# Performance work log

Hardware: AMD Instinct MI355X
Metric: run time of the kernel (lower is better)

Reference implementation:

```python
import jax, jax.numpy as jnp
import numpy as np

B, N = 1, 6
CIN, CIMG, DD = 256, 80, 59
FH, FW, IH, IW = 32, 88, 256, 704
XY0, DXY, NX = -54.0, 0.3, 360
Z0, DZ, NZ = -10.0, 20.0, 1
NPTS = B * N * DD * FH * FW


def _conv(x, w, stride, pad, b=None):
    y = jax.lax.conv_general_dilated(x, w, (stride, stride), ((pad, pad), (pad, pad)),
                                     dimension_numbers=('NCHW', 'OIHW', 'NCHW'))
    return y if b is None else y + b[None, :, None, None]


def _bnrelu(x, s, t):
    # eval-mode BatchNorm folded into per-channel scale/shift, then ReLU
    return jax.nn.relu(x * s[None, :, None, None] + t[None, :, None, None])


def _frustum():
    ds = jnp.arange(1.0, 60.0, 1.0)                      # D = 59 depth bins
    xs = jnp.linspace(0.0, IW - 1.0, FW)
    ys = jnp.linspace(0.0, IH - 1.0, FH)
    dm = jnp.broadcast_to(ds[:, None, None], (DD, FH, FW))
    xm = jnp.broadcast_to(xs[None, None, :], (DD, FH, FW))
    ym = jnp.broadcast_to(ys[None, :, None], (DD, FH, FW))
    return jnp.stack([xm, ym, dm], -1)                   # [D,FH,FW,3]


def _fwd(x_img, d, cam2lidar_rots, cam2lidar_trans, intrins, post_rots, post_trans,
         dt1_w, dt1_b, dt1_s, dt1_t, dt2_w, dt2_b, dt2_s, dt2_t, dt3_w, dt3_b, dt3_s, dt3_t,
         dn1_w, dn1_b, dn1_s, dn1_t, dn2_w, dn2_b, dn2_s, dn2_t, dn3_w, dn3_b,
         ds1_w, ds1_s, ds1_t, ds2_w, ds2_s, ds2_t):
    # ---- get_cam_feats: dtransform on raw depth, concat, depthnet ----
    h = _bnrelu(_conv(d.reshape(B * N, 1, IH, IW), dt1_w, 1, 0, dt1_b), dt1_s, dt1_t)
    h = _bnrelu(_conv(h, dt2_w, 4, 2, dt2_b), dt2_s, dt2_t)
    h = _bnrelu(_conv(h, dt3_w, 2, 2, dt3_b), dt3_s, dt3_t)      # [BN,64,FH,FW]
    f = jnp.concatenate([h, x_img], 1)                           # [BN,320,FH,FW]
    f = _bnrelu(_conv(f, dn1_w, 1, 1, dn1_b), dn1_s, dn1_t)
    f = _bnrelu(_conv(f, dn2_w, 1, 1, dn2_b), dn2_s, dn2_t)
    f = _conv(f, dn3_w, 1, 0, dn3_b)                             # [BN,D+C,FH,FW]
    depth = jax.nn.softmax(f[:, :DD], axis=1)                    # [BN,D,FH,FW]
    cam = depth[:, None] * f[:, DD:DD + CIMG][:, :, None]        # [BN,C,D,FH,FW]
    cam = cam.reshape(B, N, CIMG, DD, FH, FW).transpose(0, 1, 3, 4, 5, 2)  # [B,N,D,FH,FW,C]
    # ---- get_geometry ----
    fr = _frustum()
    pts = fr[None, None] - post_trans[:, :, None, None, None, :]
    pts = jnp.einsum('bnij,bndhwj->bndhwi', jnp.linalg.inv(post_rots), pts)
    pts = jnp.concatenate([pts[..., :2] * pts[..., 2:3], pts[..., 2:3]], -1)
    comb = jnp.einsum('bnij,bnjk->bnik', cam2lidar_rots, jnp.linalg.inv(intrins))
    pts = jnp.einsum('bnij,bndhwj->bndhwi', comb, pts) + cam2lidar_trans[:, :, None, None, None, :]
    # ---- bev_pool: voxelize + scatter-sum ----
    lo = jnp.array([XY0, XY0, Z0], dtype=pts.dtype)
    dxv = jnp.array([DXY, DXY, DZ], dtype=pts.dtype)
    g = ((pts - lo) / dxv).astype(jnp.int32).reshape(-1, 3)      # trunc-toward-zero like torch .long()
    feats = cam.reshape(-1, CIMG)
    kept = (g[:, 0] >= 0) & (g[:, 0] < NX) & (g[:, 1] >= 0) & (g[:, 1] < NX) & (g[:, 2] >= 0) & (g[:, 2] < NZ)
    bix = jnp.repeat(jnp.arange(B), NPTS // B)
    flat = ((bix * NZ + g[:, 2]) * NX + g[:, 0]) * NX + g[:, 1]
    flat = jnp.where(kept, flat, 0)
    feats = jnp.where(kept[:, None], feats, jnp.zeros((), feats.dtype))
    pooled = jax.ops.segment_sum(feats, flat, num_segments=B * NZ * NX * NX)
    # [B,Z,X,Y,C] -> [B,Z*C,X,Y] (z-major channel concat, matches cat(unbind(dim=2)))
    bev = pooled.reshape(B, NZ, NX, NX, CIMG).transpose(0, 1, 4, 2, 3).reshape(B, NZ * CIMG, NX, NX)
    # ---- downsample block (stride 2) ----
    y = _bnrelu(_conv(bev, ds1_w, 2, 1), ds1_s, ds1_t)
    y = _bnrelu(_conv(y, ds2_w, 1, 1), ds2_s, ds2_t)             # [B,80,180,180]
    return y


def setup_inputs() -> dict:
    k = jax.random.split(jax.random.key(0), 40)
    w = lambda i, s: (0.05 * jax.random.normal(k[i], s)).astype(jnp.float32)
    sc = lambda i, c: (1.0 + 0.01 * jax.random.normal(k[i], (c,))).astype(jnp.float32)
    eye = jnp.broadcast_to(jnp.eye(3, dtype=jnp.float32), (B, N, 3, 3))
    Rcl = jnp.broadcast_to(jnp.array([[0., 0., 1.], [-1., 0., 0.], [0., -1., 0.]], dtype=jnp.float32), (B, N, 3, 3))
    K = jnp.broadcast_to(jnp.array([[560., 0., 352.], [0., 560., 128.], [0., 0., 1.]], dtype=jnp.float32), (B, N, 3, 3))
    return dict(
        x_img=jax.random.normal(k[0], (B * N, CIN, FH, FW), dtype=jnp.float32),
        d=60.0 * jax.random.uniform(k[1], (B, N, 1, IH, IW), dtype=jnp.float32),
        cam2lidar_rots=Rcl + 0.005 * jax.random.normal(k[2], (B, N, 3, 3)),
        cam2lidar_trans=0.5 * jax.random.normal(k[3], (B, N, 3)),
        intrins=K,
        post_rots=eye + 0.001 * jax.random.normal(k[4], (B, N, 3, 3)),
        post_trans=jnp.zeros((B, N, 3), jnp.float32),
        dt1_w=w(5, (8, 1, 1, 1)), dt1_b=w(6, (8,)), dt1_s=sc(7, 8), dt1_t=w(8, (8,)),
        dt2_w=w(9, (32, 8, 5, 5)), dt2_b=w(10, (32,)), dt2_s=sc(11, 32), dt2_t=w(12, (32,)),
        dt3_w=w(13, (64, 32, 5, 5)), dt3_b=w(14, (64,)), dt3_s=sc(15, 64), dt3_t=w(16, (64,)),
        dn1_w=w(17, (256, 320, 3, 3)), dn1_b=w(18, (256,)), dn1_s=sc(19, 256), dn1_t=w(20, (256,)),
        dn2_w=w(21, (256, 256, 3, 3)), dn2_b=w(22, (256,)), dn2_s=sc(23, 256), dn2_t=w(24, (256,)),
        dn3_w=w(25, (139, 256, 1, 1)), dn3_b=w(26, (139,)),
        ds1_w=w(27, (80, 80, 3, 3)), ds1_s=sc(28, 80), ds1_t=w(29, (80,)),
        ds2_w=w(30, (80, 80, 3, 3)), ds2_s=sc(31, 80), ds2_t=w(32, (80,)),
    )


def reference(x_img, d, cam2lidar_rots, cam2lidar_trans, intrins, post_rots, post_trans,
              dt1_w, dt1_b, dt1_s, dt1_t, dt2_w, dt2_b, dt2_s, dt2_t, dt3_w, dt3_b, dt3_s, dt3_t,
              dn1_w, dn1_b, dn1_s, dn1_t, dn2_w, dn2_b, dn2_s, dn2_t, dn3_w, dn3_b,
              ds1_w, ds1_s, ds1_t, ds2_w, ds2_s, ds2_t):
    return _fwd(x_img, d, cam2lidar_rots, cam2lidar_trans, intrins, post_rots, post_trans,
                dt1_w, dt1_b, dt1_s, dt1_t, dt2_w, dt2_b, dt2_s, dt2_t, dt3_w, dt3_b, dt3_s, dt3_t,
                dn1_w, dn1_b, dn1_s, dn1_t, dn2_w, dn2_b, dn2_s, dn2_t, dn3_w, dn3_b,
                ds1_w, ds1_s, ds1_t, ds2_w, ds2_s, ds2_t)
```

## Files before the change

### kernel.cpp

```cpp
#include <hip/hip_runtime.h>
#include <math.h>

#define NCAM 6
#define IH 256
#define IW 704
#define FH 32
#define FW 88
#define DD 59
#define CIMG 80
#define NXv 360
#define PIX (FH*FW)
#define IMGPIX (IH*IW)
#define NPTS (NCAM*DD*PIX)
#define NCELLS (NXv*NXv)
#define NB 127
#define UNIT 32
#define MAXUNITS (NCELLS + NPTS/UNIT + 1)
#define GATHER_BLOCKS ((MAXUNITS + 3) / 4)

#define MPITCH 96
#define MROWS  35
#define MSLAB  (MROWS*MPITCH)

#define DP_R 260
#define DP_C 708
#define H2_R 68
#define H2_C 180

#define DSM   32400
#define DSP1  362
#define DSP2  182
#define DSC   96

typedef _Float16 f16;
typedef f16  f16x8 __attribute__((ext_vector_type(8)));
typedef float f32x4 __attribute__((ext_vector_type(4)));

#define SWZ(r, g) (((r)<<5) + (((g) ^ ((r)&3))<<3))

#define OFF_MATS 0
#define OFF_WDS1 144
#define OFF_WDT2 34704
#define OFF_WDS2 57744
#define OFF_A    115344
#define OFF_DNH  OFF_A
#define OFF_H2NH (OFF_A + 4416960)
#define OFF_Q3   OFF_A
#define OFF_Q2   (OFF_A + 4325376)
#define OFF_WT1  (OFF_A + 6905856)
#define OFF_WT2  (OFF_A + 7274496)
#define OFF_TD3  (OFF_A + 7569408)
#define OFF_B    10483344
#define OFF_WDT3 OFF_B
#define OFF_CNT    (OFF_B)
#define OFF_INCL   (OFF_B + 131072)
#define OFF_OFFS   (OFF_B + 262144)
#define OFF_CURSOR (OFF_B + 393216)
#define OFF_BSUM   (OFF_B + 524288)
#define OFF_UCNT   (OFF_B + 524480)
#define OFF_BSX    (OFF_B + 524544)
#define OFF_UNITS  (OFF_B + 525312)
#define OFF_POOLH  (OFF_B)
#define OFF_BEV1H  (OFF_B + 6289632)
#define OFF_C    12831888
#define OFF_D      13913232
#define OFF_Q1     OFF_D
#define OFF_FEATT  OFF_D
#define OFF_FLAT   (OFF_D + 1351680)
#define OFF_ORDYX  (OFF_D + 2348544)
#define OFF_ORDD   (OFF_D + 3345408)


__device__ __forceinline__ void inv3(const float* m, float* o) {
    float a=m[0],b=m[1],c=m[2],d=m[3],e=m[4],f=m[5],g=m[6],h=m[7],i=m[8];
    float A =  (e*i - f*h);
    float B = -(d*i - f*g);
    float C =  (d*h - e*g);
    float det = a*A + b*B + c*C;
    float r = 1.f/det;
    o[0]=A*r;            o[1]=-(b*i - c*h)*r; o[2]=(b*f - c*e)*r;
    o[3]=B*r;            o[4]=(a*i - c*g)*r;  o[5]=-(a*f - c*d)*r;
    o[6]=C*r;            o[7]=-(a*h - b*g)*r; o[8]=(a*e - b*d)*r;
}

__global__ void k_cam_mats(const float* __restrict__ prot, const float* __restrict__ ptran,
                           const float* __restrict__ intr, const float* __restrict__ Rcl,
                           const float* __restrict__ tcl, float* __restrict__ mats) {
    int n = threadIdx.x;
    if (n >= NCAM) return;
    float P[9], Km[9], R[9], A[9], Ki[9];
    for (int i=0;i<9;i++){ P[i]=prot[n*9+i]; Km[i]=intr[n*9+i]; R[i]=Rcl[n*9+i]; }
    inv3(P, A); inv3(Km, Ki);
    float* M = mats + n*24;
    for (int i=0;i<9;i++) M[i] = A[i];
    for (int r=0;r<3;r++)
        M[9+r] = -(A[r*3+0]*ptran[n*3+0] + A[r*3+1]*ptran[n*3+1] + A[r*3+2]*ptran[n*3+2]);
    for (int r=0;r<3;r++) for (int c=0;c<3;c++)
        M[12 + r*3+c] = R[r*3+0]*Ki[0*3+c] + R[r*3+1]*Ki[1*3+c] + R[r*3+2]*Ki[2*3+c];
    for (int r=0;r<3;r++) M[21+r] = tcl[n*3+r];
}

__global__ void k_wtrans_ds(const float* __restrict__ w, f16* __restrict__ Wt) {
    int i = blockIdx.x*blockDim.x + threadIdx.x;
    if (i >= 3*80*288) return;
    int k  = i % 288;
    int co = (i / 288) % 80;
    int kx = i / (288*80);
    int ky = k / 96, ci = k % 96;
    Wt[i] = (ci < 80) ? (f16)w[((co*80 + ci)*3 + kx)*3 + ky] : (f16)0.f;
}

__global__ void k_wtrans_dt2(const float* __restrict__ w, f16* __restrict__ Wt) {
    int i = blockIdx.x*blockDim.x + threadIdx.x;
    if (i >= 5*32*64) return;
    int ky = i / (32*64);
    int r  = i % (32*64);
    int co = r / 64;
    int k  = r % 64;
    int kx = k / 8, ci = k % 8;
    Wt[i] = (kx < 5) ? (f16)w[co*200 + ci*25 + ky*5 + kx] : (f16)0.f;
}

__global__ void k_wtrans_dt3(const float* __restrict__ w, f16* __restrict__ Wt) {
    int i = blockIdx.x*blockDim.x + threadIdx.x;
    if (i >= 5*64*160) return;
    int ky = i / (64*160);
    int r  = i % (64*160);
    int co = r / 160;
    int k  = r % 160;
    int kx = k / 32, ci = k % 32;
    Wt[i] = (f16)w[co*800 + ci*25 + ky*5 + kx];
}

__global__ void k_prep_b3(const float* __restrict__ w, f16* __restrict__ Wt) {
    int i = blockIdx.x*blockDim.x + threadIdx.x;
    if (i >= 144*256) return;
    int co = i / 256;
    Wt[i] = (co < 139) ? (f16)w[i] : (f16)0.f;
}

template<int CIN>
__global__ void k_prep_b(const float* __restrict__ w, f16* __restrict__ Wt) {
    int co = blockIdx.x;
    int ci = threadIdx.x;
    const float* src = w + ((size_t)co*CIN + ci)*9;
    #pragma unroll
    for (int t=0;t<9;t++)
        Wt[((size_t)t*256 + co)*CIN + ci] = (f16)src[t];
}

__global__ __launch_bounds__(256) void k_prep_d(const float* __restrict__ d,
                                                const float* __restrict__ w,
                                                const float* __restrict__ b,
                                                const float* __restrict__ s,
                                                const float* __restrict__ t,
                                                f16* __restrict__ dNH) {
    int i = blockIdx.x*256 + threadIdx.x;
    int cam = i / IMGPIX;
    int yx = i % IMGPIX;
    int y = yx / IW, x = yx % IW;
    float v = d[i];
    f16* dst = dNH + ((size_t)cam*DP_R + (y+2))*DP_C*8 + (size_t)(x+2)*8;
    #pragma unroll
    for (int c=0;c<8;c++)
        dst[c] = (f16)fmaxf(fmaf(fmaf(v, w[c], b[c]), s[c], t[c]), 0.f);
}

__global__ __launch_bounds__(256) void k_gemm_dt2(const f16* __restrict__ dNH,
                                                  const f16* __restrict__ Wt,
                                                  const float* __restrict__ bias,
                                                  const float* __restrict__ bn_s,
                                                  const float* __restrict__ bn_t,
                                                  f16* __restrict__ h2NH) {
    __shared__ f16 lA[128*32];
    __shared__ f16 lB[32*32];
    int cam = blockIdx.x / 88, mt = blockIdx.x % 88;
    int m0 = mt*128;
    int tid = threadIdx.x;
    int wid = tid>>6, lane = tid&63;
    int wm = wid*32;
    int lr = lane&15, quad = lane>>4;
    int swr = ((quad ^ (lr&3))<<3);
    f32x4 acc[2][2] = {};

    int rr = tid >> 1;
    int g0 = tid & 1, g1 = g0 + 2;
    int am = m0 + rr;
    int ay = am / 176, ax = am % 176;
    const f16* abase = dNH + (size_t)cam*DP_R*DP_C*8 + (size_t)(ay*4)*DP_C*8 + (size_t)(ax*4)*8;

    for (int ky=0; ky<5; ky++) {
        const f16* arow = abase + (size_t)ky*DP_C*8;
        const f16* brow = Wt + ((size_t)ky*32 + rr)*64;
        #pragma unroll
        for (int k0=0; k0<64; k0+=32) {
            *(float4*)(&lA[SWZ(rr,g0)]) = *(const float4*)(arow + k0 + g0*8);
            *(float4*)(&lA[SWZ(rr,g1)]) = *(const float4*)(arow + k0 + g1*8);
            if (tid < 64) {
                *(float4*)(&lB[SWZ(rr,g0)]) = *(const float4*)(brow + k0 + g0*8);
                *(float4*)(&lB[SWZ(rr,g1)]) = *(const float4*)(brow + k0 + g1*8);
            }
            __syncthreads();
            f16x8 af[2], bf[2];
            #pragma unroll
            for (int i=0;i<2;i++) af[i] = *(f16x8*)(&lA[((wm+i*16+lr)<<5) + swr]);
            #pragma unroll
            for (int j=0;j<2;j++) bf[j] = *(f16x8*)(&lB[((j*16+lr)<<5) + swr]);
            #pragma unroll
            for (int i=0;i<2;i++)
                #pragma unroll
                for (int j=0;j<2;j++)
                    acc[i][j] = __builtin_amdgcn_mfma_f32_16x16x32_f16(af[i], bf[j], acc[i][j], 0,0,0);
            __syncthreads();
        }
    }
    #pragma unroll
    for (int j=0;j<2;j++) {
        int n = j*16 + lr;
        float bb = bias[n], ss = bn_s[n], tt = bn_t[n];
        #pragma unroll
        for (int i=0;i<2;i++) {
            #pragma unroll
            for (int r=0;r<4;r++) {
                int m = m0 + wm + i*16 + quad*4 + r;
                int y = m / 176, x = m % 176;
                float v = fmaxf(fmaf(acc[i][j][r] + bb, ss, tt), 0.f);
                h2NH[((size_t)cam*H2_R + (y+2))*H2_C*32 + (size_t)(x+2)*32 + n] = (f16)v;
            }
        }
    }
}

__global__ __launch_bounds__(256) void k_gemm_dt3(const f16* __restrict__ h2NH,
                                                  const f16* __restrict__ Wt,
                                                  const float* __restrict__ bias,
                                                  const float* __restrict__ bn_s,
                                                  const float* __restrict__ bn_t,
                                                  f16* __restrict__ Q1) {
    __shared__ f16 lA[128*32];
    __shared__ f16 lB[64*32];
    int cam = blockIdx.x / 22, mt = blockIdx.x % 22;
    int m0 = mt*128;
    int tid = threadIdx.x;
    int wid = tid>>6, lane = tid&63;
    int wm = wid*32;
    int lr = lane&15, quad = lane>>4;
    int swr = ((quad ^ (lr&3))<<3);
    f32x4 acc[2][4] = {};

    int rr = tid >> 1;
    int g0 = tid & 1, g1 = g0 + 2;
    int am = m0 + rr;
    int ay = am / FW, ax = am % FW;
    const f16* abase = h2NH + (size_t)cam*H2_R*H2_C*32 + (size_t)(ay*2)*H2_C*32 + (size_t)(ax*2)*32;

    for (int ky=0; ky<5; ky++) {
        const f16* arow = abase + (size_t)ky*H2_C*32;
        const f16* brow = Wt + ((size_t)ky*64 + rr)*160;
        #pragma unroll
        for (int k0=0; k0<160; k0+=32) {
            *(float4*)(&lA[SWZ(rr,g0)]) = *(const float4*)(arow + k0 + g0*8);
            *(float4*)(&lA[SWZ(rr,g1)]) = *(const float4*)(arow + k0 + g1*8);
            if (tid < 128) {
                *(float4*)(&lB[SWZ(rr,g0)]) = *(const float4*)(brow + k0 + g0*8);
                *(float4*)(&lB[SWZ(rr,g1)]) = *(const float4*)(brow + k0 + g1*8);
            }
            __syncthreads();
            f16x8 af[2], bf[4];
            #pragma unroll
            for (int i=0;i<2;i++) af[i] = *(f16x8*)(&lA[((wm+i*16+lr)<<5) + swr]);
            #pragma unroll
            for (int j=0;j<4;j++) bf[j] = *(f16x8*)(&lB[((j*16+lr)<<5) + swr]);
            #pragma unroll
            for (int i=0;i<2;i++)
                #pragma unroll
                for (int j=0;j<4;j++)
                    acc[i][j] = __builtin_amdgcn_mfma_f32_16x16x32_f16(af[i], bf[j], acc[i][j], 0,0,0);
            __syncthreads();
        }
    }
    #pragma unroll
    for (int j=0;j<4;j++) {
        int n = j*16 + lr;
        float bb = bias[n], ss = bn_s[n], tt = bn_t[n];
        #pragma unroll
        for (int i=0;i<2;i++) {
            #pragma unroll
            for (int r=0;r<4;r++) {
                int m = m0 + wm + i*16 + quad*4 + r;
                int y = m / FW, x = m % FW;
                float v = fmaxf(fmaf(acc[i][j][r] + bb, ss, tt), 0.f);
                Q1[((size_t)cam*MSLAB + (size_t)(y+1)*MPITCH + (x+1))*320 + n] = (f16)v;
            }
        }
    }
}

__global__ __launch_bounds__(256) void k_prep_a1x(const float* __restrict__ x_img,
                                                  f16* __restrict__ Q1) {
    __shared__ f16 tile[88*260];
    int y = blockIdx.x, cam = blockIdx.y;
    for (int e = threadIdx.x; e < 88*256; e += 256) {
        int c = e / 88, p = e % 88;
        tile[p*260 + c] = (f16)x_img[((size_t)cam*256 + c)*PIX + y*FW + p];
    }
    __syncthreads();
    f16* dst = Q1 + (size_t)cam*(MSLAB*320) + ((size_t)(y+1)*MPITCH + 1)*320 + 64;
    for (int e = threadIdx.x; e < 88*256; e += 256) {
        int p = e / 256, c = e % 256;
        dst[(size_t)p*320 + c] = tile[p*260 + c];
    }
}

template<int KCI, int EPI>
__global__ __launch_bounds__(256) void k_gemm_conv(const f16* __restrict__ Aq,
                                                   const f16* __restrict__ Wt,
                                                   const float* __restrict__ bias,
                                                   const float* __restrict__ bn_s,
                                                   const float* __restrict__ bn_t,
                                                   f16* __restrict__ outh) {
    __shared__ f16 lA[128*32];
    __shared__ f16 lB[128*32];
    int cam = blockIdx.x / 24, mt = blockIdx.x % 24;
    int m0 = mt*128;
    int co0 = blockIdx.y * 128;
    int tid = threadIdx.x;
    f32x4 acc[4][4] = {};
    const f16* Abase = Aq + (size_t)cam*MSLAB*KCI;
    int rr = tid >> 1;
    int g0 = tid & 1, g1 = g0 + 2;
    int wid = tid>>6, lane = tid&63;
    int wm = (wid&1)*64, wn = (wid>>1)*64;
    int lr = lane&15, quad = lane>>4;
    int swr = ((quad ^ (lr&3))<<3);

    for (int t=0; t<9; t++) {
        int moff = (t/3)*MPITCH + (t%3);
        const f16* At = Abase + (size_t)(m0 + moff + rr)*KCI;
        const f16* Bt = Wt + ((size_t)t*256 + co0 + rr)*KCI;
        for (int k0=0; k0<KCI; k0+=32) {
            *(float4*)(&lA[SWZ(rr,g0)]) = *(const float4*)(At + k0 + g0*8);
            *(float4*)(&lA[SWZ(rr,g1)]) = *(const float4*)(At + k0 + g1*8);
            *(float4*)(&lB[SWZ(rr,g0)]) = *(const float4*)(Bt + k0 + g0*8);
            *(float4*)(&lB[SWZ(rr,g1)]) = *(const float4*)(Bt + k0 + g1*8);
            __syncthreads();
            f16x8 af[4], bf[4];
            #pragma unroll
            for (int i=0;i<4;i++) af[i] = *(f16x8*)(&lA[((wm+i*16+lr)<<5) + swr]);
            #pragma unroll
            for (int j=0;j<4;j++) bf[j] = *(f16x8*)(&lB[((wn+j*16+lr)<<5) + swr]);
            #pragma unroll
            for (int i=0;i<4;i++)
                #pragma unroll
                for (int j=0;j<4;j++)
                    acc[i][j] = __builtin_amdgcn_mfma_f32_16x16x32_f16(af[i], bf[j], acc[i][j], 0,0,0);
            __syncthreads();
        }
    }
    #pragma unroll
    for (int j=0;j<4;j++) {
        int n = co0 + wn + j*16 + lr;
        float bb = bias[n], ss = bn_s[n], tt = bn_t[n];
        #pragma unroll
        for (int i=0;i<4;i++) {
            #pragma unroll
            for (int r=0;r<4;r++) {
                int m = m0 + wm + i*16 + quad*4 + r;
                int y = m / MPITCH, x = m % MPITCH;
                if (x >= FW || y >= FH) continue;
                float v = fmaxf(fmaf(acc[i][j][r] + bb, ss, tt), 0.f);
                if (EPI == 0)
                    outh[((size_t)cam*MSLAB + (size_t)(y+1)*MPITCH + (x+1))*256 + n] = (f16)v;
                else
                    outh[((size_t)cam*PIX + (size_t)(y*FW + x))*256 + n] = (f16)v;
            }
        }
    }
}

__global__ __launch_bounds__(256) void k_gemm_dn3(const f16* __restrict__ Q3,
                                                  const f16* __restrict__ Wt,
                                                  const float* __restrict__ bias,
                                                  float* __restrict__ f3) {
    __shared__ f16 lA[128*32];
    __shared__ f16 lB[144*32];
    int cam = blockIdx.x / 22, mt = blockIdx.x % 22;
    int m0 = mt*128;
    int tid = threadIdx.x;
    int wid = tid>>6, lane = tid&63;
    int wm = wid*32;
    int lr = lane&15, quad = lane>>4;
    int swr = ((quad ^ (lr&3))<<3);
    f32x4 acc[2][9] = {};

    int rr = tid >> 1;
    int g0 = tid & 1, g1 = g0 + 2;
    const f16* abase = Q3 + ((size_t)cam*PIX + m0 + rr)*256;
    const f16* bbase = Wt + (size_t)tid*256;

    for (int k0=0; k0<256; k0+=32) {
        *(float4*)(&lA[SWZ(rr,g0)]) = *(const float4*)(abase + k0 + g0*8);
        *(float4*)(&lA[SWZ(rr,g1)]) = *(const float4*)(abase + k0 + g1*8);
        if (tid < 144) {
            #pragma unroll
            for (int g=0; g<4; g++)
                *(float4*)(&lB[SWZ(tid,g)]) = *(const float4*)(bbase + k0 + g*8);
        }
        __syncthreads();
        f16x8 af[2], bf[9];
        #pragma unroll
        for (int i=0;i<2;i++) af[i] = *(f16x8*)(&lA[((wm+i*16+lr)<<5) + swr]);
        #pragma unroll
        for (int j=0;j<9;j++) bf[j] = *(f16x8*)(&lB[((j*16+lr)<<5) + swr]);
        #pragma unroll
        for (int i=0;i<2;i++)
            #pragma unroll
            for (int j=0;j<9;j++)
                acc[i][j] = __builtin_amdgcn_mfma_f32_16x16x32_f16(af[i], bf[j], acc[i][j], 0,0,0);
        __syncthreads();
    }
    #pragma unroll
    for (int j=0;j<9;j++) {
        int n = j*16 + lr;
        if (n >= 139) continue;
        float bb = bias[n];
        #pragma unroll
        for (int i=0;i<2;i++) {
            #pragma unroll
            for (int r=0;r<4;r++) {
                int m = m0 + wm + i*16 + quad*4 + r;
                f3[((size_t)cam*139 + n)*PIX + m] = acc[i][j][r] + bb;
            }
        }
    }
}

__global__ __launch_bounds__(256) void k_softmax_feat(const float* __restrict__ f3,
                                                      float* __restrict__ depth,
                                                      float* __restrict__ featT) {
    int o = blockIdx.x*256 + threadIdx.x;
    int n = o / PIX, yx = o % PIX;
    const float* fp = f3 + (size_t)n*139*PIX + yx;
    float m = -1e30f;
    for (int d=0; d<DD; d++) m = fmaxf(m, fp[(size_t)d*PIX]);
    float sum = 0.f;
    for (int d=0; d<DD; d++) sum += expf(fp[(size_t)d*PIX]-m);
    float inv = 1.f/sum;
    for (int d=0; d<DD; d++)
        depth[((size_t)n*DD+d)*PIX + yx] = expf(fp[(size_t)d*PIX]-m)*inv;
    float* ft = featT + (size_t)o*CIMG;
    for (int c=0; c<CIMG; c++) ft[c] = fp[(size_t)(DD+c)*PIX];
}

__global__ __launch_bounds__(256) void k_voxel(const float* __restrict__ mats, int* __restrict__ flat,
                                               int* __restrict__ cnt) {
    int p = blockIdx.x*256 + threadIdx.x;
    if (p >= NPTS) return;
    int x = p % FW; int t1 = p / FW;
    int y = t1 % FH; int t2 = t1 / FH;
    int dd = t2 % DD; int n = t2 / DD;
    float xf = x * (703.f/87.f);
    float yf = y * (255.f/31.f);
    float df = 1.f + (float)dd;
    const float* M = mats + n*24;
    float qx = M[0]*xf + M[1]*yf + M[2]*df + M[9];
    float qy = M[3]*xf + M[4]*yf + M[5]*df + M[10];
    float qz = M[6]*xf + M[7]*yf + M[8]*df + M[11];
    float rx = qx*qz, ry = qy*qz, rz = qz;
    float wx = M[12]*rx + M[13]*ry + M[14]*rz + M[21];
    float wy = M[15]*rx + M[16]*ry + M[17]*rz + M[22];
    float wz = M[18]*rx + M[19]*ry + M[20]*rz + M[23];
    int gx = (int)((wx + 54.f) / 0.3f);
    int gy = (int)((wy + 54.f) / 0.3f);
    int gz = (int)((wz + 10.f) / 20.f);
    bool kept = ((unsigned)gx < NXv) && ((unsigned)gy < NXv) && (gz == 0);
    int cell = kept ? (gx*NXv + gy) : -1;
    flat[p] = cell;
    if (kept) atomicAdd(&cnt[cell], 1);
}

__global__ __launch_bounds__(256) void k_scan1(const int* __restrict__ cnt, int* __restrict__ incl,
                                               int* __restrict__ bsum) {
    int tid = threadIdx.x;
    int idx = blockIdx.x*1024 + tid*4;
    int c0 = (idx+0 < NCELLS) ? cnt[idx+0] : 0;
    int c1 = (idx+1 < NCELLS) ? cnt[idx+1] : 0;
    int c2 = (idx+2 < NCELLS) ? cnt[idx+2] : 0;
    int c3 = (idx+3 < NCELLS) ? cnt[idx+3] : 0;
    int s0=c0, s1=s0+c1, s2=s1+c2, s3=s2+c3;
    int v = s3;
    int lane = tid & 63, wid = tid >> 6;
    #pragma unroll
    for (int d=1; d<64; d<<=1) {
        int u = __shfl_up(v, d, 64);
        if (lane >= d) v += u;
    }
    __shared__ int wsum[4];
    if (lane == 63) wsum[wid] = v;
    __syncthreads();
    int woff = 0;
    #pragma unroll
    for (int w=0; w<3; w++) if (w < wid) woff += wsum[w];
    int texcl = woff + v - s3;
    if (idx+0 < NCELLS) incl[idx+0] = texcl + s0;
    if (idx+1 < NCELLS) incl[idx+1] = texcl + s1;
    if (idx+2 < NCELLS) incl[idx+2] = texcl + s2;
    if (idx+3 < NCELLS) incl[idx+3] = texcl + s3;
    if (tid == 255) bsum[blockIdx.x] = woff + v;
}

__global__ void k_scan2(const int* __restrict__ bsum, int* __restrict__ bsx,
                        int* __restrict__ ucount) {
    int lane = threadIdx.x;
    if (lane == 0) *ucount = 0;
    int a = (2*lane   < NB) ? bsum[2*lane]   : 0;
    int b = (2*lane+1 < NB) ? bsum[2*lane+1] : 0;
    int s = a + b;
    int v = s;
    #pragma unroll
    for (int d=1; d<64; d<<=1) {
        int u = __shfl_up(v, d, 64);
        if (lane >= d) v += u;
    }
    int excl = v - s;
    if (2*lane   < NB) bsx[2*lane]   = excl;
    if (2*lane+1 < NB) bsx[2*lane+1] = excl + a;
}

__global__ __launch_bounds__(256) void k_scan3(const int* __restrict__ incl, const int* __restrict__ cnt,
                                               const int* __restrict__ bsx, int* __restrict__ offs,
                                               int* __restrict__ cursor,
                                               int* __restrict__ units, int* __restrict__ ucount) {
    int idx = blockIdx.x*1024 + threadIdx.x*4;
    int o = bsx[blockIdx.x];
    #pragma unroll
    for (int j=0;j<4;j++) {
        int cell = idx + j;
        if (cell < NCELLS) {
            int k = cnt[cell];
            int e = o + incl[cell] - k;
            offs[cell] = e;
            cursor[cell] = e;
            if (k > 0) {
                int nu = (k + UNIT-1) / UNIT;
                int ub = atomicAdd(ucount, nu);
                int multi = (nu > 1) ? (1<<17) : 0;
                for (int u=0; u<nu; u++) {
                    int c2 = min(UNIT, k - u*UNIT);
                    units[2*(ub+u)]   = cell | multi | (c2<<18);
                    units[2*(ub+u)+1] = e + u*UNIT;
                }
            }
        }
    }
}

__global__ __launch_bounds__(256) void k_fill(const int* __restrict__ flat, int* __restrict__ cursor,
                                              const float* __restrict__ depth,
                                              int* __restrict__ ordYX, float* __restrict__ ordD) {
    int p = blockIdx.x*256 + threadIdx.x;
    if (p >= NPTS) return;
    int cell = flat[p];
    if (cell < 0) return;
    int pos = atomicAdd(&cursor[cell], 1);
    int n = p / (DD*PIX);
    int yx = p % PIX;
    ordYX[pos] = n*PIX + yx;
    ordD[pos] = depth[p];
}

__global__ __launch_bounds__(256) void k_gather2(const int* __restrict__ units,
                                                 const int* __restrict__ ucount,
                                                 const int* __restrict__ ordYX,
                                                 const float* __restrict__ ordD,
                                                 const float* __restrict__ featT,
                                                 float* __restrict__ pooled) {
    int idx = blockIdx.x*4 + (threadIdx.x >> 6);
    if (idx >= *ucount) return;
    int lane = threadIdx.x & 63;
    int u0 = units[2*idx], base = units[2*idx+1];
    int cell = u0 & 0x1ffff;
    bool multi = (u0 >> 17) & 1;
    int count = u0 >> 18;
    float acc0 = 0.f, acc1 = 0.f;
    bool lo = (lane < 16);
    int i = 0;
    for (; i+2 <= count; i += 2) {
        int y0 = ordYX[base+i], y1 = ordYX[base+i+1];
        float d0 = ordD[base+i], d1 = ordD[base+i+1];
        const float* f0 = featT + (size_t)y0*CIMG;
        const float* f1 = featT + (size_t)y1*CIMG;
        float a = f0[lane];
        float b = f1[lane];
        float c = lo ? f0[64+lane] : 0.f;
        float d = lo ? f1[64+lane] : 0.f;
        acc0 = fmaf(d0, a, acc0);
        acc0 = fmaf(d1, b, acc0);
        acc1 = fmaf(d0, c, acc1);
        acc1 = fmaf(d1, d, acc1);
    }
    if (i < count) {
        int y0 = ordYX[base+i];
        float d0 = ordD[base+i];
        const float* f0 = featT + (size_t)y0*CIMG;
        acc0 = fmaf(d0, f0[lane], acc0);
        if (lo) acc1 = fmaf(d0, f0[64+lane], acc1);
    }
    float* dst = pooled + (size_t)cell*CIMG;
    if (multi) {
        atomicAdd(dst + lane, acc0);
        if (lo) atomicAdd(dst + 64 + lane, acc1);
    } else {
        dst[lane] = acc0;
        if (lo) dst[64 + lane] = acc1;
    }
}

__global__ __launch_bounds__(256) void k_pool2h(const float* __restrict__ pooled,
                                                f16* __restrict__ pooledH) {
    int gx = blockIdx.x;
    const float* src = pooled + (size_t)gx*360*80;
    for (int e = threadIdx.x; e < 360*80; e += 256) {
        int gy = e / 80, c = e % 80;
        pooledH[((size_t)(gx+1)*DSP1 + (gy+1))*DSC + c] = (f16)src[e];
    }
}

template<int STRIDE, int HINP, int EPI>
__global__ __launch_bounds__(256) void k_ds_mfma(const f16* __restrict__ inH,
                                                 const f16* __restrict__ Wt,
                                                 const float* __restrict__ bn_s,
                                                 const float* __restrict__ bn_t,
                                                 f16* __restrict__ outh,
                                                 float* __restrict__ outf) {
    __shared__ f16 lA[128*32];
    __shared__ f16 lB[80*32];
    int m0 = blockIdx.x * 128;
    int tid = threadIdx.x;
    int wid = tid>>6, lane = tid&63;
    int wm = wid*32;
    int lr = lane&15, quad = lane>>4;
    int swr = ((quad ^ (lr&3))<<3);
    f32x4 acc[2][5] = {};

    int rr = tid >> 1;
    int g0 = tid & 1, g1 = g0 + 2;
    int am = min(m0 + rr, DSM-1);
    int axo = am / 180, ayo = am % 180;
    const f16* arow0 = inH + ((size_t)(axo*STRIDE)*HINP + (size_t)ayo*STRIDE)*DSC;
    const f16* brow0 = Wt + (size_t)rr*288;

    for (int kx=0; kx<3; kx++) {
        const f16* arow = arow0 + (size_t)kx*HINP*DSC;
        const f16* brow = brow0 + (size_t)kx*80*288;
        for (int k0=0; k0<288; k0+=32) {
            *(float4*)(&lA[SWZ(rr,g0)]) = *(const float4*)(arow + k0 + g0*8);
            *(float4*)(&lA[SWZ(rr,g1)]) = *(const float4*)(arow + k0 + g1*8);
            if (tid < 160) {
                *(float4*)(&lB[SWZ(rr,g0)]) = *(const float4*)(brow + k0 + g0*8);
                *(float4*)(&lB[SWZ(rr,g1)]) = *(const float4*)(brow + k0 + g1*8);
            }
            __syncthreads();
            f16x8 af[2], bf[5];
            #pragma unroll
            for (int i=0;i<2;i++) af[i] = *(f16x8*)(&lA[((wm+i*16+lr)<<5) + swr]);
            #pragma unroll
            for (int j=0;j<5;j++) bf[j] = *(f16x8*)(&lB[((j*16+lr)<<5) + swr]);
            #pragma unroll
            for (int i=0;i<2;i++)
                #pragma unroll
                for (int j=0;j<5;j++)
                    acc[i][j] = __builtin_amdgcn_mfma_f32_16x16x32_f16(af[i], bf[j], acc[i][j], 0,0,0);
            __syncthreads();
        }
    }
    #pragma unroll
    for (int j=0;j<5;j++) {
        int n = j*16 + lr;
        float ss = bn_s[n], tt = bn_t[n];
        #pragma unroll
        for (int i=0;i<2;i++) {
            #pragma unroll
            for (int r=0;r<4;r++) {
                int m = m0 + wm + i*16 + quad*4 + r;
                if (m >= DSM) continue;
                float v = fmaxf(fmaf(acc[i][j][r], ss, tt), 0.f);
                if (EPI == 0) {
                    int xo = m / 180, yo = m % 180;
                    outh[((size_t)(xo+1)*DSP2 + (yo+1))*DSC + n] = (f16)v;
                } else {
                    outf[(size_t)n*DSM + m] = v;
                }
            }
        }
    }
}

extern "C" void kernel_launch(void* const* d_in, const int* in_sizes, int n_in,
                              void* d_out, int out_size, void* d_ws, size_t ws_size,
                              hipStream_t stream) {
    const float* x_img  = (const float*)d_in[0];
    const float* dimg   = (const float*)d_in[1];
    const float* c2l_R  = (const float*)d_in[2];
    const float* c2l_t  = (const float*)d_in[3];
    const float* intr   = (const float*)d_in[4];
    const float* prot   = (const float*)d_in[5];
    const float* ptran  = (const float*)d_in[6];
    const float* dt1_w  = (const float*)d_in[7];
    const float* dt1_b  = (const float*)d_in[8];
    const float* dt1_s  = (const float*)d_in[9];
    const float* dt1_t  = (const float*)d_in[10];
    const float* dt2_w  = (const float*)d_in[11];
    const float* dt2_b  = (const float*)d_in[12];
    const float* dt2_s  = (const float*)d_in[13];
    const float* dt2_t  = (const float*)d_in[14];
    const float* dt3_w  = (const float*)d_in[15];
    const float* dt3_b  = (const float*)d_in[16];
    const float* dt3_s  = (const float*)d_in[17];
    const float* dt3_t  = (const float*)d_in[18];
    const float* dn1_w  = (const float*)d_in[19];
    const float* dn1_b  = (const float*)d_in[20];
    const float* dn1_s  = (const float*)d_in[21];
    const float* dn1_t  = (const float*)d_in[22];
    const float* dn2_w  = (const float*)d_in[23];
    const float* dn2_b  = (const float*)d_in[24];
    const float* dn2_s  = (const float*)d_in[25];
    const float* dn2_t  = (const float*)d_in[26];
    const float* dn3_w  = (const float*)d_in[27];
    const float* dn3_b  = (const float*)d_in[28];
    const float* ds1_w  = (const float*)d_in[29];
    const float* ds1_s  = (const float*)d_in[30];
    const float* ds1_t  = (const float*)d_in[31];
    const float* ds2_w  = (const float*)d_in[32];
    const float* ds2_s  = (const float*)d_in[33];
    const float* ds2_t  = (const float*)d_in[34];

    float* ws = (float*)d_ws;
    float* mats   = ws + OFF_MATS;
    f16*   WtDS1  = (f16*)(ws + OFF_WDS1);
    f16*   WtDS2  = (f16*)(ws + OFF_WDS2);
    f16*   WtDT2  = (f16*)(ws + OFF_WDT2);
    f16*   WtDT3  = (f16*)(ws + OFF_WDT3);
    f16*   dNH    = (f16*)(ws + OFF_DNH);
    f16*   h2NH   = (f16*)(ws + OFF_H2NH);
    f16*   Q3     = (f16*)(ws + OFF_Q3);
    float* pooled = ws + OFF_A;
    f16*   Q2     = (f16*)(ws + OFF_Q2);
    f16*   Wt1    = (f16*)(ws + OFF_WT1);
    f16*   Wt2    = (f16*)(ws + OFF_WT2);
    f16*   Wt3h   = (f16*)(ws + OFF_TD3);
    float* f3     = ws + OFF_B;
    int*   cnt    = (int*)(ws + OFF_CNT);
    int*   incl   = (int*)(ws + OFF_INCL);
    int*   offs   = (int*)(ws + OFF_OFFS);
    int*   cursor = (int*)(ws + OFF_CURSOR);
    int*   bsum   = (int*)(ws + OFF_BSUM);
    int*   ucnt   = (int*)(ws + OFF_UCNT);
    int*   bsx    = (int*)(ws + OFF_BSX);
    int*   units  = (int*)(ws + OFF_UNITS);
    f16*   pooledH= (f16*)(ws + OFF_POOLH);
    f16*   bev1H  = (f16*)(ws + OFF_BEV1H);
    float* depth  = ws + OFF_C;
    f16*   Q1     = (f16*)(ws + OFF_Q1);
    float* featT  = ws + OFF_FEATT;
    int*   flat   = (int*)(ws + OFF_FLAT);
    int*   ordYX  = (int*)(ws + OFF_ORDYX);
    float* ordD   = ws + OFF_ORDD;
    float* outp   = (float*)d_out;

    k_cam_mats<<<1, 64, 0, stream>>>(prot, ptran, intr, c2l_R, c2l_t, mats);
    k_wtrans_ds<<<270, 256, 0, stream>>>(ds1_w, WtDS1);
    k_wtrans_ds<<<270, 256, 0, stream>>>(ds2_w, WtDS2);
    k_wtrans_dt2<<<40, 256, 0, stream>>>(dt2_w, WtDT2);
    k_wtrans_dt3<<<200, 256, 0, stream>>>(dt3_w, WtDT3);
    k_prep_b3<<<144, 256, 0, stream>>>(dn3_w, Wt3h);
    k_prep_b<320><<<256, 320, 0, stream>>>(dn1_w, Wt1);
    k_prep_b<256><<<256, 256, 0, stream>>>(dn2_w, Wt2);

    hipMemsetAsync(dNH, 0, (size_t)NCAM*DP_R*DP_C*8*sizeof(f16), stream);
    hipMemsetAsync(h2NH, 0, (size_t)NCAM*H2_R*H2_C*32*sizeof(f16), stream);
    hipMemsetAsync(Q1, 0, (size_t)NCAM*MSLAB*320*sizeof(f16), stream);

    k_prep_d<<<4224, 256, 0, stream>>>(dimg, dt1_w, dt1_b, dt1_s, dt1_t, dNH);
    k_gemm_dt2<<<528, 256, 0, stream>>>(dNH, WtDT2, dt2_b, dt2_s, dt2_t, h2NH);
    k_gemm_dt3<<<132, 256, 0, stream>>>(h2NH, WtDT3, dt3_b, dt3_s, dt3_t, Q1);
    k_prep_a1x<<<dim3(32,NCAM), 256, 0, stream>>>(x_img, Q1);

    hipMemsetAsync(Q2, 0, (size_t)NCAM*MSLAB*256*sizeof(f16), stream);
    k_gemm_conv<320,0><<<dim3(144,2), 256, 0, stream>>>(Q1, Wt1, dn1_b, dn1_s, dn1_t, Q2);
    k_gemm_conv<256,1><<<dim3(144,2), 256, 0, stream>>>(Q2, Wt2, dn2_b, dn2_s, dn2_t, Q3);
    k_gemm_dn3<<<132, 256, 0, stream>>>(Q3, Wt3h, dn3_b, f3);

    k_softmax_feat<<<66, 256, 0, stream>>>(f3, depth, featT);

    hipMemsetAsync(cnt, 0, NCELLS*sizeof(int), stream);
    hipMemsetAsync(pooled, 0, (size_t)NCELLS*CIMG*sizeof(float), stream);
    k_voxel<<<3894, 256, 0, stream>>>(mats, flat, cnt);
    k_scan1<<<NB, 256, 0, stream>>>(cnt, incl, bsum);
    k_scan2<<<1, 64, 0, stream>>>(bsum, bsx, ucnt);
    k_scan3<<<NB, 256, 0, stream>>>(incl, cnt, bsx, offs, cursor, units, ucnt);
    k_fill<<<3894, 256, 0, stream>>>(flat, cursor, depth, ordYX, ordD);
    k_gather2<<<GATHER_BLOCKS, 256, 0, stream>>>(units, ucnt, ordYX, ordD, featT, pooled);

    hipMemsetAsync(pooledH, 0, (size_t)DSP1*DSP1*DSC*sizeof(f16), stream);
    hipMemsetAsync(bev1H, 0, (size_t)DSP2*DSP2*DSC*sizeof(f16), stream);
    k_pool2h<<<360, 256, 0, stream>>>(pooled, pooledH);
    k_ds_mfma<2,DSP1,0><<<254, 256, 0, stream>>>(pooledH, WtDS1, ds1_s, ds1_t, bev1H, nullptr);
    k_ds_mfma<1,DSP2,1><<<254, 256, 0, stream>>>(bev1H, WtDS2, ds2_s, ds2_t, nullptr, outp);
}
```

Baseline: 691.0 us.

## Split softmax and feature transpose; store transposed features in fp16 for gather

Splits the fused softmax/feature-copy kernel in two. The softmax now keeps the 59 depth logits in registers, so it reads f3 once instead of three times and computes exp once. A new shared-memory tiled transpose kernel writes the image features as fp16 with coalesced reads and writes, replacing the strided per-thread copy. The gather kernel reads these half-precision features, which halves its random-access traffic, at the cost of reduced feature precision before pooling.

```diff
diff --git a/kernel.cpp b/kernel.cpp
--- a/kernel.cpp
+++ b/kernel.cpp
@@ -70,7 +70,6 @@
 #define OFF_ORDYX  (OFF_D + 2348544)
 #define OFF_ORDD   (OFF_D + 3345408)
 
-
 __device__ __forceinline__ void inv3(const float* m, float* o) {
     float a=m[0],b=m[1],c=m[2],d=m[3],e=m[4],f=m[5],g=m[6],h=m[7],i=m[8];
     float A =  (e*i - f*h);
@@ -435,21 +434,41 @@
     }
 }
 
-__global__ __launch_bounds__(256) void k_softmax_feat(const float* __restrict__ f3,
-                                                      float* __restrict__ depth,
-                                                      float* __restrict__ featT) {
+__global__ __launch_bounds__(256) void k_softmax2(const float* __restrict__ f3,
+                                                  float* __restrict__ depth) {
     int o = blockIdx.x*256 + threadIdx.x;
     int n = o / PIX, yx = o % PIX;
     const float* fp = f3 + (size_t)n*139*PIX + yx;
+    float r[DD];
+    #pragma unroll
+    for (int d=0; d<DD; d++) r[d] = fp[(size_t)d*PIX];
     float m = -1e30f;
-    for (int d=0; d<DD; d++) m = fmaxf(m, fp[(size_t)d*PIX]);
+    #pragma unroll
+    for (int d=0; d<DD; d++) m = fmaxf(m, r[d]);
     float sum = 0.f;
-    for (int d=0; d<DD; d++) sum += expf(fp[(size_t)d*PIX]-m);
+    #pragma unroll
+    for (int d=0; d<DD; d++) { r[d] = expf(r[d]-m); sum += r[d]; }
     float inv = 1.f/sum;
+    #pragma unroll
     for (int d=0; d<DD; d++)
-        depth[((size_t)n*DD+d)*PIX + yx] = expf(fp[(size_t)d*PIX]-m)*inv;
-    float* ft = featT + (size_t)o*CIMG;
-    for (int c=0; c<CIMG; c++) ft[c] = fp[(size_t)(DD+c)*PIX];
+        depth[((size_t)n*DD+d)*PIX + yx] = r[d]*inv;
+}
+
+__global__ __launch_bounds__(256) void k_featT(const float* __restrict__ f3,
+                                               f16* __restrict__ featTh) {
+    __shared__ float tile[88*81];
+    int y = blockIdx.x, cam = blockIdx.y;
+    const float* src = f3 + (size_t)cam*139*PIX + (size_t)DD*PIX + y*FW;
+    for (int e = threadIdx.x; e < 88*80; e += 256) {
+        int c = e / 88, p = e % 88;
+        tile[p*81 + c] = src[(size_t)c*PIX + p];
+    }
+    __syncthreads();
+    f16* dst = featTh + ((size_t)cam*PIX + y*FW)*CIMG;
+    for (int e = threadIdx.x; e < 88*80; e += 256) {
+        int p = e / 80, c = e % 80;
+        dst[(size_t)p*CIMG + c] = (f16)tile[p*81 + c];
+    }
 }
 
 __global__ __launch_bounds__(256) void k_voxel(const float* __restrict__ mats, int* __restrict__ flat,
@@ -573,7 +592,7 @@
                                                  const int* __restrict__ ucount,
                                                  const int* __restrict__ ordYX,
                                                  const float* __restrict__ ordD,
-                                                 const float* __restrict__ featT,
+                                                 const f16* __restrict__ featTh,
                                                  float* __restrict__ pooled) {
     int idx = blockIdx.x*4 + (threadIdx.x >> 6);
     if (idx >= *ucount) return;
@@ -588,12 +607,12 @@
     for (; i+2 <= count; i += 2) {
         int y0 = ordYX[base+i], y1 = ordYX[base+i+1];
         float d0 = ordD[base+i], d1 = ordD[base+i+1];
-        const float* f0 = featT + (size_t)y0*CIMG;
-        const float* f1 = featT + (size_t)y1*CIMG;
-        float a = f0[lane];
-        float b = f1[lane];
-        float c = lo ? f0[64+lane] : 0.f;
-        float d = lo ? f1[64+lane] : 0.f;
+        const f16* f0 = featTh + (size_t)y0*CIMG;
+        const f16* f1 = featTh + (size_t)y1*CIMG;
+        float a = (float)f0[lane];
+        float b = (float)f1[lane];
+        float c = lo ? (float)f0[64+lane] : 0.f;
+        float d = lo ? (float)f1[64+lane] : 0.f;
         acc0 = fmaf(d0, a, acc0);
         acc0 = fmaf(d1, b, acc0);
         acc1 = fmaf(d0, c, acc1);
@@ -602,9 +621,9 @@
     if (i < count) {
         int y0 = ordYX[base+i];
         float d0 = ordD[base+i];
-        const float* f0 = featT + (size_t)y0*CIMG;
-        acc0 = fmaf(d0, f0[lane], acc0);
-        if (lo) acc1 = fmaf(d0, f0[64+lane], acc1);
+        const f16* f0 = featTh + (size_t)y0*CIMG;
+        acc0 = fmaf(d0, (float)f0[lane], acc0);
+        if (lo) acc1 = fmaf(d0, (float)f0[64+lane], acc1);
     }
     float* dst = pooled + (size_t)cell*CIMG;
     if (multi) {
@@ -762,7 +781,7 @@
     f16*   bev1H  = (f16*)(ws + OFF_BEV1H);
     float* depth  = ws + OFF_C;
     f16*   Q1     = (f16*)(ws + OFF_Q1);
-    float* featT  = ws + OFF_FEATT;
+    f16*   featTh = (f16*)(ws + OFF_FEATT);
     int*   flat   = (int*)(ws + OFF_FLAT);
     int*   ordYX  = (int*)(ws + OFF_ORDYX);
     float* ordD   = ws + OFF_ORDD;
@@ -791,7 +810,8 @@
     k_gemm_conv<256,1><<<dim3(144,2), 256, 0, stream>>>(Q2, Wt2, dn2_b, dn2_s, dn2_t, Q3);
     k_gemm_dn3<<<132, 256, 0, stream>>>(Q3, Wt3h, dn3_b, f3);
 
-    k_softmax_feat<<<66, 256, 0, stream>>>(f3, depth, featT);
+    k_softmax2<<<66, 256, 0, stream>>>(f3, depth);
+    k_featT<<<dim3(32,NCAM), 256, 0, stream>>>(f3, featTh);
 
     hipMemsetAsync(cnt, 0, NCELLS*sizeof(int), stream);
     hipMemsetAsync(pooled, 0, (size_t)NCELLS*CIMG*sizeof(float), stream);
@@ -800,7 +820,7 @@
     k_scan2<<<1, 64, 0, stream>>>(bsum, bsx, ucnt);
     k_scan3<<<NB, 256, 0, stream>>>(incl, cnt, bsx, offs, cursor, units, ucnt);
     k_fill<<<3894, 256, 0, stream>>>(flat, cursor, depth, ordYX, ordD);
-    k_gather2<<<GATHER_BLOCKS, 256, 0, stream>>>(units, ucnt, ordYX, ordD, featT, pooled);
+    k_gather2<<<GATHER_BLOCKS, 256, 0, stream>>>(units, ucnt, ordYX, ordD, featTh, pooled);
 
     hipMemsetAsync(pooledH, 0, (size_t)DSP1*DSP1*DSC*sizeof(f16), stream);
     hipMemsetAsync(bev1H, 0, (size_t)DSP2*DSP2*DSC*sizeof(f16), stream);
```

Result: no change. 695.8 us (+0.7%).
